# Performance work log

Hardware: AMD Instinct MI355X
Metric: run time of the kernel (lower is better)

The kernel has to match this reference:

```python
import jax, jax.numpy as jnp
import numpy as np

N_NODES = 100000
N_EDGES = 1600000
IN_DIM = 128
HID = 128
OUT = 112


def setup_inputs() -> dict:
    key = jax.random.key(0)
    ks = jax.random.split(key, 8)
    s = 1.0 / np.sqrt(IN_DIM)
    sh = 1.0 / np.sqrt(HID)
    return {
        "x": jax.random.normal(ks[0], (N_NODES, IN_DIM), jnp.float32),
        "edge_index": jax.random.randint(ks[1], (2, N_EDGES), 0, N_NODES, jnp.int64),
        "W_l1": jax.random.normal(ks[2], (HID, IN_DIM), jnp.float32) * s,
        "b_l1": jnp.zeros((HID,), jnp.float32),
        "W_r1": jax.random.normal(ks[3], (HID, IN_DIM), jnp.float32) * s,
        "W_l2": jax.random.normal(ks[4], (HID, HID), jnp.float32) * sh,
        "b_l2": jnp.zeros((HID,), jnp.float32),
        "W_r2": jax.random.normal(ks[5], (HID, HID), jnp.float32) * sh,
        "W_out": jax.random.normal(ks[6], (OUT, HID), jnp.float32) * sh,
        "b_out": jnp.zeros((OUT,), jnp.float32),
    }


def _sage_conv(x, edge_index, W_l, b_l, W_r):
    # PyG SAGEConv, aggr='mean', root_weight=True:
    #   out_i = W_l @ mean_{j in N(i)} x_j + b_l + W_r @ x_i
    src, dst = edge_index[0], edge_index[1]
    n = x.shape[0]
    agg = jax.ops.segment_sum(x[src], dst, num_segments=n)          # [N, d]
    deg = jax.ops.segment_sum(jnp.ones_like(dst, dtype=x.dtype), dst, num_segments=n)
    mean = agg / jnp.maximum(deg, 1.0)[:, None]
    return mean @ W_l.T + b_l + x @ W_r.T


def reference(x, edge_index, W_l1, b_l1, W_r1, W_l2, b_l2, W_r2, W_out, b_out):
    h = jax.nn.relu(_sage_conv(x, edge_index, W_l1, b_l1, W_r1))
    # dropout p=0.2 is identity at inference (training=False)
    h = jax.nn.relu(_sage_conv(h, edge_index, W_l2, b_l2, W_r2))
    return h @ W_out.T + b_out  # [N, 112] logits
```

## Files before the change

kernel.cpp:

```cpp
#include <hip/hip_runtime.h>
#include <hip/hip_bf16.h>

#define HID 128
#define OUT_DIM 112
#define CAP 4096

typedef short bf16x8 __attribute__((ext_vector_type(8)));
typedef float f32x4 __attribute__((ext_vector_type(4)));

__device__ __forceinline__ ushort f2b(float f) {
  __hip_bfloat16 h = __float2bfloat16(f);
  return *reinterpret_cast<ushort*>(&h);
}
__device__ __forceinline__ float blo(uint u) { return __uint_as_float(u << 16); }
__device__ __forceinline__ float bhi(uint u) { return __uint_as_float(u & 0xffff0000u); }

__global__ __launch_bounds__(256) void f2b_kernel(
    const float* __restrict__ in, ushort* __restrict__ out, int n4) {
  int i = blockIdx.x * 256 + threadIdx.x;
  if (i >= n4) return;
  float4 v = ((const float4*)in)[i];
  ushort4 r;
  r.x = f2b(v.x); r.y = f2b(v.y); r.z = f2b(v.z); r.w = f2b(v.w);
  ((ushort4*)out)[i] = r;
}

__global__ __launch_bounds__(256) void packw_all_kernel(
    const float* __restrict__ Wl1, const float* __restrict__ Wr1,
    const float* __restrict__ Wl2, const float* __restrict__ Wr2,
    const float* __restrict__ Wo, ushort* __restrict__ WB1,
    ushort* __restrict__ WB2, ushort* __restrict__ WBO) {
  int p = blockIdx.x * 256 + threadIdx.x;
  const float* W;
  ushort* wb;
  int ntiles, off;
  if (p < 16384)      { W = Wl1; wb = WB1;         ntiles = 8; off = p; }
  else if (p < 32768) { W = Wr1; wb = WB1 + 16384; ntiles = 8; off = p - 16384; }
  else if (p < 49152) { W = Wl2; wb = WB2;         ntiles = 8; off = p - 32768; }
  else if (p < 65536) { W = Wr2; wb = WB2 + 16384; ntiles = 8; off = p - 49152; }
  else if (p < 79872) { W = Wo;  wb = WBO;         ntiles = 7; off = p - 65536; }
  else return;
  int j = off & 7;
  int l = (off >> 3) & 63;
  int rest = off >> 9;
  int nt = rest % ntiles;
  int ks = rest / ntiles;
  int nn = nt * 16 + (l & 15);
  int k = ks * 32 + (l >> 4) * 8 + j;
  wb[off] = f2b(W[nn * 128 + k]);
}

__global__ __launch_bounds__(256) void hist_kernel(
    const int* __restrict__ dst, int* __restrict__ gcount, int e, int nb) {
  __shared__ int lh[1024];
  const int t = threadIdx.x;
  for (int i = t; i < nb; i += 256) lh[i] = 0;
  __syncthreads();
  int base = blockIdx.x * 4096;
#pragma unroll
  for (int j = 0; j < 16; ++j) {
    int i = base + j * 256 + t;
    if (i < e) atomicAdd(&lh[dst[i] >> 7], 1);
  }
  __syncthreads();
  for (int i = t; i < nb; i += 256)
    if (lh[i]) atomicAdd(&gcount[i], lh[i]);
}

__global__ __launch_bounds__(1024) void scan_nb_kernel(
    const int* __restrict__ gcount, int* __restrict__ gbase,
    int* __restrict__ gcursor, int* __restrict__ rowstart,
    int e, int n, int nb) {
  __shared__ int wsum[16];
  const int t = threadIdx.x, lane = t & 63, wid = t >> 6;
  int v = (t < nb) ? gcount[t] : 0;
  int s = v;
#pragma unroll
  for (int off = 1; off < 64; off <<= 1) {
    int u = __shfl_up(s, off, 64);
    if (lane >= off) s += u;
  }
  if (lane == 63) wsum[wid] = s;
  __syncthreads();
  if (wid == 0) {
    int ws = (lane < 16) ? wsum[lane] : 0;
#pragma unroll
    for (int off = 1; off < 16; off <<= 1) {
      int u = __shfl_up(ws, off, 64);
      if (lane >= off) ws += u;
    }
    if (lane < 16) wsum[lane] = ws;
  }
  __syncthreads();
  int excl = s - v + (wid ? wsum[wid - 1] : 0);
  if (t < nb) {
    gbase[t] = excl;
    gcursor[t] = excl;
  }
  if (t == 0) {
    gbase[nb] = e;
    rowstart[n] = e;
  }
}

__global__ __launch_bounds__(1024) void bucket_scatter_kernel(
    const int* __restrict__ src, const int* __restrict__ dst,
    int* __restrict__ gcursor, uint* __restrict__ bedges, int e, int nb) {
  __shared__ int lh[1024];
  __shared__ int lstart[1024];
  __shared__ int wsum[16];
  __shared__ uint sp[8192];
  __shared__ ushort sb[8192];
  const int t = threadIdx.x, lane = t & 63, wid = t >> 6;
  const int base = blockIdx.x * 8192;
  const int ecnt = min(8192, e - base);
  for (int i = t; i < nb; i += 1024) lh[i] = 0;
  __syncthreads();
  int myb[8], myr[8];
  uint myp[8];
#pragma unroll
  for (int j = 0; j < 8; ++j) {
    int i = base + j * 1024 + t;
    myb[j] = -1;
    if (i < e) {
      int d = dst[i];
      int sv = src[i];
      int b = d >> 7;
      myb[j] = b;
      myp[j] = ((uint)sv << 7) | (uint)(d & 127);
      myr[j] = atomicAdd(&lh[b], 1);
    }
  }
  __syncthreads();
  int cnt = (t < nb) ? lh[t] : 0;
  int s = cnt;
#pragma unroll
  for (int off = 1; off < 64; off <<= 1) {
    int u = __shfl_up(s, off, 64);
    if (lane >= off) s += u;
  }
  if (lane == 63) wsum[wid] = s;
  __syncthreads();
  if (wid == 0) {
    int ws = (lane < 16) ? wsum[lane] : 0;
#pragma unroll
    for (int off = 1; off < 16; off <<= 1) {
      int u = __shfl_up(ws, off, 64);
      if (lane >= off) ws += u;
    }
    if (lane < 16) wsum[lane] = ws;
  }
  __syncthreads();
  int excl = s - cnt + (wid ? wsum[wid - 1] : 0);
  if (t < nb) lstart[t] = excl;
  __syncthreads();
  if (t < nb) lh[t] = (cnt > 0) ? atomicAdd(&gcursor[t], cnt) : 0;
  __syncthreads();
#pragma unroll
  for (int j = 0; j < 8; ++j) {
    if (myb[j] >= 0) {
      int slot = lstart[myb[j]] + myr[j];
      sp[slot] = myp[j];
      sb[slot] = (ushort)myb[j];
    }
  }
  __syncthreads();
#pragma unroll
  for (int j = 0; j < 8; ++j) {
    int i = j * 1024 + t;
    if (i < ecnt) {
      int b = sb[i];
      int pos = lh[b] + (i - lstart[b]);
      bedges[pos] = sp[i];
    }
  }
}

__global__ __launch_bounds__(256) void csr_build_kernel(
    const uint* __restrict__ bedges, const int* __restrict__ gbase,
    int* __restrict__ rowstart, float* __restrict__ dinv,
    int* __restrict__ csr_src, int n) {
  __shared__ int lh[128];
  __shared__ int lst[128];
  __shared__ int lcur[128];
  __shared__ int wsum2[4];
  __shared__ int lsorted[CAP];
  const int t = threadIdx.x;
  const int bkt = blockIdx.x;
  const int node0 = bkt << 7;
  const int g0 = gbase[bkt], g1 = gbase[bkt + 1];
  const int cnt = g1 - g0;
  if (t < 128) lh[t] = 0;
  __syncthreads();
  for (int i = t; i < cnt; i += 256)
    atomicAdd(&lh[bedges[g0 + i] & 127], 1);
  __syncthreads();
  const int lane = t & 63, wid = t >> 6;
  int v = (t < 128) ? lh[t] : 0;
  int s = v;
#pragma unroll
  for (int off = 1; off < 64; off <<= 1) {
    int u = __shfl_up(s, off, 64);
    if (lane >= off) s += u;
  }
  if (t < 128 && lane == 63) wsum2[wid] = s;
  __syncthreads();
  int excl = s - v + ((wid == 1) ? wsum2[0] : 0);
  if (t < 128) {
    lst[t] = excl;
    lcur[t] = excl;
    int node = node0 + t;
    if (node < n) {
      rowstart[node] = g0 + excl;
      dinv[node] = 1.0f / (float)max(v, 1);
    }
  }
  __syncthreads();
  for (int i = t; i < cnt; i += 256) {
    uint p = bedges[g0 + i];
    int d = p & 127;
    int slot = atomicAdd(&lcur[d], 1);
    int sv = (int)(p >> 7);
    if (slot < CAP) lsorted[slot] = sv;
    else csr_src[g0 + slot] = sv;
  }
  __syncthreads();
  int lim = min(cnt, CAP);
  for (int i = t; i < lim; i += 256) csr_src[g0 + i] = lsorted[i];
}

__global__ __launch_bounds__(256) void agg_bf16_kernel(
    const ushort* __restrict__ xb, const int* __restrict__ csr_src,
    const int* __restrict__ rowstart, const float* __restrict__ dinv,
    ushort* __restrict__ aggb, int n) {
  int node = blockIdx.x * 4 + (threadIdx.x >> 6);
  int lane = threadIdx.x & 63;
  if (node >= n) return;
  int s = rowstart[node], e1 = rowstart[node + 1];
  const int c = lane & 15;
  const int eslot = lane >> 4;
  float a0 = 0.f, a1 = 0.f, a2 = 0.f, a3 = 0.f;
  float a4 = 0.f, a5 = 0.f, a6 = 0.f, a7 = 0.f;
#pragma unroll 2
  for (int e = s + eslot; e < e1; e += 4) {
    int sv = csr_src[e];
    uint4 u = ((const uint4*)(xb + (size_t)sv * 128))[c];
    a0 += blo(u.x); a1 += bhi(u.x);
    a2 += blo(u.y); a3 += bhi(u.y);
    a4 += blo(u.z); a5 += bhi(u.z);
    a6 += blo(u.w); a7 += bhi(u.w);
  }
  a0 += __shfl_xor(a0, 16, 64); a1 += __shfl_xor(a1, 16, 64);
  a2 += __shfl_xor(a2, 16, 64); a3 += __shfl_xor(a3, 16, 64);
  a4 += __shfl_xor(a4, 16, 64); a5 += __shfl_xor(a5, 16, 64);
  a6 += __shfl_xor(a6, 16, 64); a7 += __shfl_xor(a7, 16, 64);
  a0 += __shfl_xor(a0, 32, 64); a1 += __shfl_xor(a1, 32, 64);
  a2 += __shfl_xor(a2, 32, 64); a3 += __shfl_xor(a3, 32, 64);
  a4 += __shfl_xor(a4, 32, 64); a5 += __shfl_xor(a5, 32, 64);
  a6 += __shfl_xor(a6, 32, 64); a7 += __shfl_xor(a7, 32, 64);
  if (eslot == 0) {
    float sc = dinv[node];
    uint4 r;
    r.x = (uint)f2b(a0 * sc) | ((uint)f2b(a1 * sc) << 16);
    r.y = (uint)f2b(a2 * sc) | ((uint)f2b(a3 * sc) << 16);
    r.z = (uint)f2b(a4 * sc) | ((uint)f2b(a5 * sc) << 16);
    r.w = (uint)f2b(a6 * sc) | ((uint)f2b(a7 * sc) << 16);
    ((uint4*)(aggb + (size_t)node * 128))[c] = r;
  }
}

__global__ __launch_bounds__(256) void lin_mfma_kernel(
    const ushort* __restrict__ meanb, const ushort* __restrict__ xb,
    const ushort* __restrict__ wb, const float* __restrict__ bias,
    ushort* __restrict__ outb, int n) {
  __shared__ ushort zA[64 * 128];
  __shared__ ushort zX[64 * 128];
  const int t = threadIdx.x;
  const int block0 = blockIdx.x * 64;
#pragma unroll
  for (int i = 0; i < 4; ++i) {
    int c = i * 256 + t;
    int row = c >> 4;
    int col = c & 15;
    int node = block0 + row;
    int4 va = make_int4(0, 0, 0, 0), vx = make_int4(0, 0, 0, 0);
    if (node < n) {
      va = ((const int4*)(meanb + (size_t)node * 128))[col];
      vx = ((const int4*)(xb + (size_t)node * 128))[col];
    }
    ((int4*)zA)[c] = va;
    ((int4*)zX)[c] = vx;
  }
  __syncthreads();
  const int lane = t & 63;
  const int wave = t >> 6;
  const int m0 = wave * 16;
  const int cidx = lane & 15;
  const int quad = lane >> 4;
  f32x4 acc[8];
#pragma unroll
  for (int nt = 0; nt < 8; ++nt) acc[nt] = (f32x4){0.f, 0.f, 0.f, 0.f};
#pragma unroll
  for (int s = 0; s < 2; ++s) {
    const ushort* zs = (s == 0) ? zA : zX;
#pragma unroll
    for (int ks = 0; ks < 4; ++ks) {
      bf16x8 a = *(const bf16x8*)(zs + (m0 + cidx) * 128 + ks * 32 + quad * 8);
      const ushort* wp = wb + ((size_t)((s * 4 + ks) * 8) * 64 + lane) * 8;
#pragma unroll
      for (int nt = 0; nt < 8; ++nt) {
        bf16x8 b = *(const bf16x8*)(wp + nt * 512);
        acc[nt] = __builtin_amdgcn_mfma_f32_16x16x32_bf16(a, b, acc[nt], 0, 0, 0);
      }
    }
  }
  __syncthreads();
#pragma unroll
  for (int nt = 0; nt < 8; ++nt) {
    float bv = bias[nt * 16 + cidx];
#pragma unroll
    for (int i = 0; i < 4; ++i) {
      float v = fmaxf(acc[nt][i] + bv, 0.f);
      zA[(m0 + quad * 4 + i) * 128 + nt * 16 + cidx] = f2b(v);
    }
  }
  __syncthreads();
#pragma unroll
  for (int i = 0; i < 4; ++i) {
    int c = i * 256 + t;
    int row = c >> 4;
    int col = c & 15;
    int node = block0 + row;
    if (node < n) ((int4*)(outb + (size_t)node * 128))[col] = ((const int4*)zA)[c];
  }
}

__global__ __launch_bounds__(256) void out_mfma_kernel(
    const ushort* __restrict__ h2b, const ushort* __restrict__ wb,
    const float* __restrict__ bias, float* __restrict__ outp, int n) {
  __shared__ ushort zt[64 * 128];
  __shared__ float zo[64 * 112];
  const int t = threadIdx.x;
  const int block0 = blockIdx.x * 64;
#pragma unroll
  for (int i = 0; i < 4; ++i) {
    int c = i * 256 + t;
    int row = c >> 4;
    int col = c & 15;
    int node = block0 + row;
    int4 v = make_int4(0, 0, 0, 0);
    if (node < n) v = ((const int4*)(h2b + (size_t)node * 128))[col];
    ((int4*)zt)[c] = v;
  }
  __syncthreads();
  const int lane = t & 63;
  const int wave = t >> 6;
  const int m0 = wave * 16;
  const int cidx = lane & 15;
  const int quad = lane >> 4;
  f32x4 acc[7];
#pragma unroll
  for (int nt = 0; nt < 7; ++nt) acc[nt] = (f32x4){0.f, 0.f, 0.f, 0.f};
#pragma unroll
  for (int ks = 0; ks < 4; ++ks) {
    bf16x8 a = *(const bf16x8*)(zt + (m0 + cidx) * 128 + ks * 32 + quad * 8);
    const ushort* wp = wb + ((size_t)(ks * 7) * 64 + lane) * 8;
#pragma unroll
    for (int nt = 0; nt < 7; ++nt) {
      bf16x8 b = *(const bf16x8*)(wp + nt * 512);
      acc[nt] = __builtin_amdgcn_mfma_f32_16x16x32_bf16(a, b, acc[nt], 0, 0, 0);
    }
  }
#pragma unroll
  for (int nt = 0; nt < 7; ++nt) {
    float bv = bias[nt * 16 + cidx];
#pragma unroll
    for (int i = 0; i < 4; ++i)
      zo[(m0 + quad * 4 + i) * 112 + nt * 16 + cidx] = acc[nt][i] + bv;
  }
  __syncthreads();
#pragma unroll
  for (int i = 0; i < 7; ++i) {
    int c = i * 256 + t;
    int node = block0 + c / 28;
    if (node < n)
      ((float4*)(outp + (size_t)block0 * 112))[c] = ((const float4*)zo)[c];
  }
}

extern "C" void kernel_launch(void* const* d_in, const int* in_sizes, int n_in,
                              void* d_out, int out_size, void* d_ws, size_t ws_size,
                              hipStream_t stream) {
  const float* x     = (const float*)d_in[0];
  const int*   ei    = (const int*)d_in[1];
  const float* W_l1  = (const float*)d_in[2];
  const float* b_l1  = (const float*)d_in[3];
  const float* W_r1  = (const float*)d_in[4];
  const float* W_l2  = (const float*)d_in[5];
  const float* b_l2  = (const float*)d_in[6];
  const float* W_r2  = (const float*)d_in[7];
  const float* W_out = (const float*)d_in[8];
  const float* b_out = (const float*)d_in[9];

  const int N = in_sizes[0] / 128;
  const int E = in_sizes[1] / 2;
  const int NB = (N + 127) >> 7;
  const int* src = ei;
  const int* dst = ei + E;

  ushort* XB = (ushort*)d_ws;
  ushort* MB = XB + (size_t)N * 128;
  ushort* HB = MB + (size_t)N * 128;
  float* DINV = (float*)(HB + (size_t)N * 128);
  ushort* WB1 = (ushort*)(DINV + N);
  ushort* WB2 = WB1 + 32768;
  ushort* WBO = WB2 + 32768;
  int* GCOUNT   = (int*)(WBO + 14336);
  int* GBASE    = GCOUNT + NB;
  int* GCURSOR  = GBASE + NB + 1;
  int* ROWSTART = GCURSOR + NB;
  uint* BEDGES  = (uint*)(ROWSTART + N + 1);
  int* CSRSRC   = (int*)(BEDGES + E);

  hipMemsetAsync(GCOUNT, 0, (size_t)NB * sizeof(int), stream);
  hist_kernel<<<(E + 4095) / 4096, 256, 0, stream>>>(dst, GCOUNT, E, NB);
  scan_nb_kernel<<<1, 1024, 0, stream>>>(GCOUNT, GBASE, GCURSOR, ROWSTART, E, N, NB);
  bucket_scatter_kernel<<<(E + 8191) / 8192, 1024, 0, stream>>>(
      src, dst, GCURSOR, BEDGES, E, NB);
  csr_build_kernel<<<NB, 256, 0, stream>>>(BEDGES, GBASE, ROWSTART, DINV, CSRSRC, N);

  int n4 = N * 128 / 4;
  f2b_kernel<<<(n4 + 255) / 256, 256, 0, stream>>>(x, XB, n4);
  packw_all_kernel<<<312, 256, 0, stream>>>(W_l1, W_r1, W_l2, W_r2, W_out,
                                            WB1, WB2, WBO);

  int ablocks = (N + 3) / 4;
  int lblocks = (N + 63) / 64;

  agg_bf16_kernel<<<ablocks, 256, 0, stream>>>(XB, CSRSRC, ROWSTART, DINV, MB, N);
  lin_mfma_kernel<<<lblocks, 256, 0, stream>>>(MB, XB, WB1, b_l1, HB, N);

  agg_bf16_kernel<<<ablocks, 256, 0, stream>>>(HB, CSRSRC, ROWSTART, DINV, MB, N);
  lin_mfma_kernel<<<lblocks, 256, 0, stream>>>(MB, HB, WB2, b_l2, XB, N);

  out_mfma_kernel<<<lblocks, 256, 0, stream>>>(XB, WBO, b_out, (float*)d_out, N);
}
```

Baseline: 342.0 us.

## Merge prep kernels, fuse layer-2 linear with output projection, unroll gather

The f2b, histogram and weight-pack kernels are merged into one launch, with block ranges selecting the role. The layer-2 linear and the output projection are fused so the hidden activations stay in shared memory instead of making a round trip through global memory. The aggregation loop now issues four independent neighbor-row loads per iteration to raise memory-level parallelism. In exchange, the fused kernel uses more shared memory and registers, which may lower occupancy.

Measured after the change: 330.1 us. 3.5% less time.

```diff
diff --git a/kernel.cpp b/kernel.cpp
--- a/kernel.cpp
+++ b/kernel.cpp
@@ -15,22 +15,42 @@
 __device__ __forceinline__ float blo(uint u) { return __uint_as_float(u << 16); }
 __device__ __forceinline__ float bhi(uint u) { return __uint_as_float(u & 0xffff0000u); }
 
-__global__ __launch_bounds__(256) void f2b_kernel(
-    const float* __restrict__ in, ushort* __restrict__ out, int n4) {
-  int i = blockIdx.x * 256 + threadIdx.x;
-  if (i >= n4) return;
-  float4 v = ((const float4*)in)[i];
-  ushort4 r;
-  r.x = f2b(v.x); r.y = f2b(v.y); r.z = f2b(v.z); r.w = f2b(v.w);
-  ((ushort4*)out)[i] = r;
-}
-
-__global__ __launch_bounds__(256) void packw_all_kernel(
+__global__ __launch_bounds__(256) void prep_kernel(
+    const float* __restrict__ x, ushort* __restrict__ xb, int n4,
+    const int* __restrict__ dst, int* __restrict__ gcount, int e, int nb,
     const float* __restrict__ Wl1, const float* __restrict__ Wr1,
     const float* __restrict__ Wl2, const float* __restrict__ Wr2,
     const float* __restrict__ Wo, ushort* __restrict__ WB1,
-    ushort* __restrict__ WB2, ushort* __restrict__ WBO) {
-  int p = blockIdx.x * 256 + threadIdx.x;
+    ushort* __restrict__ WB2, ushort* __restrict__ WBO,
+    int f2b_blocks, int hist_blocks) {
+  __shared__ int lh[1024];
+  const int b = blockIdx.x;
+  const int t = threadIdx.x;
+  if (b < f2b_blocks) {
+    int i = b * 256 + t;
+    if (i < n4) {
+      float4 v = ((const float4*)x)[i];
+      ushort4 r;
+      r.x = f2b(v.x); r.y = f2b(v.y); r.z = f2b(v.z); r.w = f2b(v.w);
+      ((ushort4*)xb)[i] = r;
+    }
+    return;
+  }
+  if (b < f2b_blocks + hist_blocks) {
+    for (int i = t; i < nb; i += 256) lh[i] = 0;
+    __syncthreads();
+    int base = (b - f2b_blocks) * 4096;
+#pragma unroll
+    for (int j = 0; j < 16; ++j) {
+      int i = base + j * 256 + t;
+      if (i < e) atomicAdd(&lh[dst[i] >> 7], 1);
+    }
+    __syncthreads();
+    for (int i = t; i < nb; i += 256)
+      if (lh[i]) atomicAdd(&gcount[i], lh[i]);
+    return;
+  }
+  int p = (b - f2b_blocks - hist_blocks) * 256 + t;
   const float* W;
   ushort* wb;
   int ntiles, off;
@@ -50,23 +70,6 @@
   wb[off] = f2b(W[nn * 128 + k]);
 }
 
-__global__ __launch_bounds__(256) void hist_kernel(
-    const int* __restrict__ dst, int* __restrict__ gcount, int e, int nb) {
-  __shared__ int lh[1024];
-  const int t = threadIdx.x;
-  for (int i = t; i < nb; i += 256) lh[i] = 0;
-  __syncthreads();
-  int base = blockIdx.x * 4096;
-#pragma unroll
-  for (int j = 0; j < 16; ++j) {
-    int i = base + j * 256 + t;
-    if (i < e) atomicAdd(&lh[dst[i] >> 7], 1);
-  }
-  __syncthreads();
-  for (int i = t; i < nb; i += 256)
-    if (lh[i]) atomicAdd(&gcount[i], lh[i]);
-}
-
 __global__ __launch_bounds__(1024) void scan_nb_kernel(
     const int* __restrict__ gcount, int* __restrict__ gbase,
     int* __restrict__ gcursor, int* __restrict__ rowstart,
@@ -241,8 +244,26 @@
   const int eslot = lane >> 4;
   float a0 = 0.f, a1 = 0.f, a2 = 0.f, a3 = 0.f;
   float a4 = 0.f, a5 = 0.f, a6 = 0.f, a7 = 0.f;
-#pragma unroll 2
-  for (int e = s + eslot; e < e1; e += 4) {
+  int e = s + eslot;
+  for (; e + 12 < e1; e += 16) {
+    int s0 = csr_src[e];
+    int s1 = csr_src[e + 4];
+    int s2 = csr_src[e + 8];
+    int s3 = csr_src[e + 12];
+    uint4 u0 = ((const uint4*)(xb + (size_t)s0 * 128))[c];
+    uint4 u1 = ((const uint4*)(xb + (size_t)s1 * 128))[c];
+    uint4 u2 = ((const uint4*)(xb + (size_t)s2 * 128))[c];
+    uint4 u3 = ((const uint4*)(xb + (size_t)s3 * 128))[c];
+    a0 += (blo(u0.x) + blo(u1.x)) + (blo(u2.x) + blo(u3.x));
+    a1 += (bhi(u0.x) + bhi(u1.x)) + (bhi(u2.x) + bhi(u3.x));
+    a2 += (blo(u0.y) + blo(u1.y)) + (blo(u2.y) + blo(u3.y));
+    a3 += (bhi(u0.y) + bhi(u1.y)) + (bhi(u2.y) + bhi(u3.y));
+    a4 += (blo(u0.z) + blo(u1.z)) + (blo(u2.z) + blo(u3.z));
+    a5 += (bhi(u0.z) + bhi(u1.z)) + (bhi(u2.z) + bhi(u3.z));
+    a6 += (blo(u0.w) + blo(u1.w)) + (blo(u2.w) + blo(u3.w));
+    a7 += (bhi(u0.w) + bhi(u1.w)) + (bhi(u2.w) + bhi(u3.w));
+  }
+  for (; e < e1; e += 4) {
     int sv = csr_src[e];
     uint4 u = ((const uint4*)(xb + (size_t)sv * 128))[c];
     a0 += blo(u.x); a1 += bhi(u.x);
@@ -335,11 +356,15 @@
   }
 }
 
-__global__ __launch_bounds__(256) void out_mfma_kernel(
-    const ushort* __restrict__ h2b, const ushort* __restrict__ wb,
-    const float* __restrict__ bias, float* __restrict__ outp, int n) {
-  __shared__ ushort zt[64 * 128];
-  __shared__ float zo[64 * 112];
+__global__ __launch_bounds__(256) void lin2out_kernel(
+    const ushort* __restrict__ meanb, const ushort* __restrict__ hb,
+    const ushort* __restrict__ wb, const float* __restrict__ bias,
+    const ushort* __restrict__ wbo, const float* __restrict__ bias_o,
+    float* __restrict__ outp, int n) {
+  __shared__ ushort smem[2 * 64 * 128];
+  ushort* zA = smem;
+  ushort* zX = smem + 64 * 128;
+  float* zo = (float*)smem;
   const int t = threadIdx.x;
   const int block0 = blockIdx.x * 64;
 #pragma unroll
@@ -348,9 +373,13 @@
     int row = c >> 4;
     int col = c & 15;
     int node = block0 + row;
-    int4 v = make_int4(0, 0, 0, 0);
-    if (node < n) v = ((const int4*)(h2b + (size_t)node * 128))[col];
-    ((int4*)zt)[c] = v;
+    int4 va = make_int4(0, 0, 0, 0), vx = make_int4(0, 0, 0, 0);
+    if (node < n) {
+      va = ((const int4*)(meanb + (size_t)node * 128))[col];
+      vx = ((const int4*)(hb + (size_t)node * 128))[col];
+    }
+    ((int4*)zA)[c] = va;
+    ((int4*)zX)[c] = vx;
   }
   __syncthreads();
   const int lane = t & 63;
@@ -358,25 +387,52 @@
   const int m0 = wave * 16;
   const int cidx = lane & 15;
   const int quad = lane >> 4;
-  f32x4 acc[7];
-#pragma unroll
-  for (int nt = 0; nt < 7; ++nt) acc[nt] = (f32x4){0.f, 0.f, 0.f, 0.f};
+  f32x4 acc[8];
+#pragma unroll
+  for (int nt = 0; nt < 8; ++nt) acc[nt] = (f32x4){0.f, 0.f, 0.f, 0.f};
+#pragma unroll
+  for (int s = 0; s < 2; ++s) {
+    const ushort* zs = (s == 0) ? zA : zX;
+#pragma unroll
+    for (int ks = 0; ks < 4; ++ks) {
+      bf16x8 a = *(const bf16x8*)(zs + (m0 + cidx) * 128 + ks * 32 + quad * 8);
+      const ushort* wp = wb + ((size_t)((s * 4 + ks) * 8) * 64 + lane) * 8;
+#pragma unroll
+      for (int nt = 0; nt < 8; ++nt) {
+        bf16x8 b = *(const bf16x8*)(wp + nt * 512);
+        acc[nt] = __builtin_amdgcn_mfma_f32_16x16x32_bf16(a, b, acc[nt], 0, 0, 0);
+      }
+    }
+  }
+#pragma unroll
+  for (int nt = 0; nt < 8; ++nt) {
+    float bv = bias[nt * 16 + cidx];
+#pragma unroll
+    for (int i = 0; i < 4; ++i) {
+      float v = fmaxf(acc[nt][i] + bv, 0.f);
+      zX[(m0 + quad * 4 + i) * 128 + nt * 16 + cidx] = f2b(v);
+    }
+  }
+  f32x4 acc2[7];
+#pragma unroll
+  for (int nt = 0; nt < 7; ++nt) acc2[nt] = (f32x4){0.f, 0.f, 0.f, 0.f};
 #pragma unroll
   for (int ks = 0; ks < 4; ++ks) {
-    bf16x8 a = *(const bf16x8*)(zt + (m0 + cidx) * 128 + ks * 32 + quad * 8);
-    const ushort* wp = wb + ((size_t)(ks * 7) * 64 + lane) * 8;
+    bf16x8 a = *(const bf16x8*)(zX + (m0 + cidx) * 128 + ks * 32 + quad * 8);
+    const ushort* wp = wbo + ((size_t)(ks * 7) * 64 + lane) * 8;
 #pragma unroll
     for (int nt = 0; nt < 7; ++nt) {
       bf16x8 b = *(const bf16x8*)(wp + nt * 512);
-      acc[nt] = __builtin_amdgcn_mfma_f32_16x16x32_bf16(a, b, acc[nt], 0, 0, 0);
-    }
-  }
+      acc2[nt] = __builtin_amdgcn_mfma_f32_16x16x32_bf16(a, b, acc2[nt], 0, 0, 0);
+    }
+  }
+  __syncthreads();
 #pragma unroll
   for (int nt = 0; nt < 7; ++nt) {
-    float bv = bias[nt * 16 + cidx];
+    float bv = bias_o[nt * 16 + cidx];
 #pragma unroll
     for (int i = 0; i < 4; ++i)
-      zo[(m0 + quad * 4 + i) * 112 + nt * 16 + cidx] = acc[nt][i] + bv;
+      zo[(m0 + quad * 4 + i) * 112 + nt * 16 + cidx] = acc2[nt][i] + bv;
   }
   __syncthreads();
 #pragma unroll
@@ -423,17 +479,21 @@
   int* CSRSRC   = (int*)(BEDGES + E);
 
   hipMemsetAsync(GCOUNT, 0, (size_t)NB * sizeof(int), stream);
-  hist_kernel<<<(E + 4095) / 4096, 256, 0, stream>>>(dst, GCOUNT, E, NB);
+
+  int n4 = N * 128 / 4;
+  int f2b_blocks = (n4 + 255) / 256;
+  int hist_blocks = (E + 4095) / 4096;
+  int packw_blocks = 312;
+  prep_kernel<<<f2b_blocks + hist_blocks + packw_blocks, 256, 0, stream>>>(
+      x, XB, n4, dst, GCOUNT, E, NB,
+      W_l1, W_r1, W_l2, W_r2, W_out, WB1, WB2, WBO,
+      f2b_blocks, hist_blocks);
+
   scan_nb_kernel<<<1, 1024, 0, stream>>>(GCOUNT, GBASE, GCURSOR, ROWSTART, E, N, NB);
   bucket_scatter_kernel<<<(E + 8191) / 8192, 1024, 0, stream>>>(
       src, dst, GCURSOR, BEDGES, E, NB);
   csr_build_kernel<<<NB, 256, 0, stream>>>(BEDGES, GBASE, ROWSTART, DINV, CSRSRC, N);
 
-  int n4 = N * 128 / 4;
-  f2b_kernel<<<(n4 + 255) / 256, 256, 0, stream>>>(x, XB, n4);
-  packw_all_kernel<<<312, 256, 0, stream>>>(W_l1, W_r1, W_l2, W_r2, W_out,
-                                            WB1, WB2, WBO);
-
   int ablocks = (N + 3) / 4;
   int lblocks = (N + 63) / 64;
 
@@ -441,7 +501,6 @@
   lin_mfma_kernel<<<lblocks, 256, 0, stream>>>(MB, XB, WB1, b_l1, HB, N);
 
   agg_bf16_kernel<<<ablocks, 256, 0, stream>>>(HB, CSRSRC, ROWSTART, DINV, MB, N);
-  lin_mfma_kernel<<<lblocks, 256, 0, stream>>>(MB, HB, WB2, b_l2, XB, N);
-
-  out_mfma_kernel<<<lblocks, 256, 0, stream>>>(XB, WBO, b_out, (float*)d_out, N);
-}
+  lin2out_kernel<<<lblocks, 256, 0, stream>>>(MB, HB, WB2, b_l2, WBO, b_out,
+                                              (float*)d_out, N);
+}
```
